# Performance work log

Hardware: AMD Instinct MI355X
Metric: run time of the kernel (lower is better)

Reference implementation:

```python
import jax, jax.numpy as jnp
import numpy as np

NUM_LAYERS = 2
DIM_Z = 128
NORM = float(np.sqrt(DIM_Z))
EPS = 1e-5


def _ln(v):
    # LayerNorm(elementwise_affine=False) over last dim
    m = v.mean(-1, keepdims=True)
    var = ((v - m) ** 2).mean(-1, keepdims=True)
    return (v - m) / jnp.sqrt(var + EPS)


def setup_inputs() -> dict:
    key = jax.random.key(0)
    ks = jax.random.split(key, 8)
    B, C, P = 32, 128, 128
    K, DS = 510, 256
    H = W = 64
    return {
        "x": jax.random.normal(ks[0], (B, C, P), jnp.float32),
        "latents": jax.random.normal(ks[1], (K, DS), jnp.float32),
        "blank_latent": jax.random.normal(ks[2], (NUM_LAYERS, DIM_Z), jnp.float32),
        "linear_w": jax.random.normal(ks[3], (DIM_Z, DS), jnp.float32) * 0.05,
        "linear_b": jnp.zeros((DIM_Z,), jnp.float32),
        "anchors_w": jax.random.normal(ks[4], (DIM_Z, C), jnp.float32) * 0.05,
        "anchors_b": jnp.zeros((DIM_Z,), jnp.float32),
        "prototypes": jax.random.uniform(ks[5], (K, 3, H, W), dtype=jnp.float32),
        "masks": jax.random.uniform(ks[6], (K, 1, H, W), dtype=jnp.float32),
    }


def reference(x, latents, blank_latent, linear_w, linear_b, anchors_w, anchors_b, prototypes, masks):
    B, C, P = x.shape
    L = NUM_LAYERS
    # codebook latents: (K, dim_sprites) -> Linear -> LN -> (K, dim_z)
    lat = _ln(latents @ linear_w.T + linear_b)
    xp = jnp.transpose(x, (0, 2, 1))                          # (B, P, C)
    a = _ln(xp.reshape(B * P, C) @ anchors_w.T + anchors_b)   # (B*P, dim_z)
    logits_main = a @ lat.T                                   # (B*P, K)
    # blank logits: position p uses blank_latent[p % L]; value repeated L times
    blank_pp = blank_latent[jnp.arange(P) % L]                # (P, dim_z == C)
    dots = jnp.einsum('bpc,pc->bp', xp, blank_pp)             # (B, P)
    logits_blank = jnp.broadcast_to(dots.reshape(B * P, 1), (B * P, L))
    logits = jnp.concatenate([logits_main, logits_blank], axis=-1) / NORM
    weights = jax.nn.softmax(logits, axis=-1)                 # (B*P, K+L)
    log_probs = jax.nn.log_softmax(
        jnp.transpose(logits.reshape(B, P, -1), (1, 0, 2)), axis=2)  # (P, B, K+L)
    # sprite bank: [prototypes;0] on rgb, [masks;0] on alpha -> (K+L, 4, H, W)
    zp = jnp.zeros((L,) + prototypes.shape[1:], prototypes.dtype)
    zm = jnp.zeros((L,) + masks.shape[1:], masks.dtype)
    sprite = jnp.concatenate(
        [jnp.concatenate([prototypes, zp], axis=0),
         jnp.concatenate([masks, zm], axis=0)], axis=1)
    # broadcast-multiply-reduce expressed as a single contraction
    S = jnp.einsum('nk,kchw->nchw', weights, sprite)          # (B*P, 4, H, W)
    H_, W_ = S.shape[-2], S.shape[-1]
    S_out = jnp.transpose(S.reshape(B, P, 4, H_, W_), (1, 0, 2, 3, 4))  # (P, B, 4, H, W)
    return (weights, logits, log_probs, S_out)
```

## Files before the change

### kernel.cpp

```cpp
#include <hip/hip_runtime.h>

typedef unsigned short u16;
typedef unsigned int u32;
typedef __bf16 bf16x8 __attribute__((ext_vector_type(8)));
typedef float f32x4 __attribute__((ext_vector_type(4)));

#define EPS 1e-5f
#define INV_NORM 0.088388347648318447f

#define OUT_W   0
#define OUT_LOG 2097152
#define OUT_LP  4194304
#define OUT_S   6291456

#define WS_BT   0
#define WS_LAT  8388608
#define WS_A    8454144

__device__ __forceinline__ u16 f2b(float f) {
  u32 i = __float_as_uint(f);
  return (u16)((i + 0x7FFFu + ((i >> 16) & 1u)) >> 16);
}
__device__ __forceinline__ float wsum(float v) {
#pragma unroll
  for (int off = 32; off > 0; off >>= 1) v += __shfl_down(v, off, 64);
  return v;
}
__device__ __forceinline__ float wmax(float v) {
#pragma unroll
  for (int off = 32; off > 0; off >>= 1) v = fmaxf(v, __shfl_down(v, off, 64));
  return v;
}
__device__ __forceinline__ float dot8(uint4 u, const float* xp) {
  float s;
  s  = xp[0] * __uint_as_float(u.x << 16);
  s += xp[1] * __uint_as_float(u.x & 0xFFFF0000u);
  s += xp[2] * __uint_as_float(u.y << 16);
  s += xp[3] * __uint_as_float(u.y & 0xFFFF0000u);
  s += xp[4] * __uint_as_float(u.z << 16);
  s += xp[5] * __uint_as_float(u.z & 0xFFFF0000u);
  s += xp[6] * __uint_as_float(u.w << 16);
  s += xp[7] * __uint_as_float(u.w & 0xFFFF0000u);
  return s;
}
__device__ __forceinline__ float dot4(float4 u, const float* xp) {
  return xp[0] * u.x + xp[1] * u.y + xp[2] * u.z + xp[3] * u.w;
}

__global__ __launch_bounds__(128) void k_lat(const float* __restrict__ latents,
                                             const float* __restrict__ lw,
                                             const float* __restrict__ lb,
                                             u16* __restrict__ latbf) {
  int k = blockIdx.x, t = threadIdx.x;
  int wid = t >> 6, lane = t & 63;
  __shared__ float ls[256];
  __shared__ float red[4];
  ls[t] = latents[k * 256 + t];
  ls[t + 128] = latents[k * 256 + 128 + t];
  __syncthreads();
  float v = lb[t];
  const float4* wv = (const float4*)(lw + t * 256);
#pragma unroll
  for (int c = 0; c < 64; c++) v += dot4(wv[c], &ls[c * 4]);
  float s = wsum(v), s2 = wsum(v * v);
  if (lane == 0) { red[wid * 2] = s; red[wid * 2 + 1] = s2; }
  __syncthreads();
  float mean = (red[0] + red[2]) * 0.0078125f;
  float var = (red[1] + red[3]) * 0.0078125f - mean * mean;
  latbf[k * 128 + t] = f2b((v - mean) * rsqrtf(var + EPS));
}

__global__ __launch_bounds__(256) void k_tr(const float* __restrict__ proto,
                                            const float* __restrict__ masks,
                                            u16* __restrict__ Bt) {
  __shared__ u16 tile[64 * 72];
  int t = threadIdx.x;
  int n0 = blockIdx.x * 64;
  int k0 = blockIdx.y * 64;
  int ch = n0 >> 12, hw0 = n0 & 4095;
  int r = t >> 2, c = (t & 3) * 16;
  int kg = k0 + r;
  u16 vals[16];
#pragma unroll
  for (int e = 0; e < 16; e++) vals[e] = 0;
  if (kg < 510) {
    const float* src = (ch < 3) ? (proto + ((size_t)kg * 3 + ch) * 4096 + hw0 + c)
                                : (masks + (size_t)kg * 4096 + hw0 + c);
    const float4* s4 = (const float4*)src;
#pragma unroll
    for (int q = 0; q < 4; q++) {
      float4 u = s4[q];
      vals[q * 4 + 0] = f2b(u.x);
      vals[q * 4 + 1] = f2b(u.y);
      vals[q * 4 + 2] = f2b(u.z);
      vals[q * 4 + 3] = f2b(u.w);
    }
  }
#pragma unroll
  for (int e = 0; e < 16; e++) tile[r * 72 + c + e] = vals[e];
  __syncthreads();
  int nr = t >> 2, kc = (t & 3) * 16;
  u32 u[8];
#pragma unroll
  for (int e = 0; e < 8; e++) {
    u32 lo = tile[(kc + 2 * e) * 72 + nr];
    u32 hi = tile[(kc + 2 * e + 1) * 72 + nr];
    u[e] = lo | (hi << 16);
  }
  u16* dst = Bt + (size_t)(n0 + nr) * 512 + k0 + kc;
  uint4 v0 = {u[0], u[1], u[2], u[3]};
  uint4 v1 = {u[4], u[5], u[6], u[7]};
  *(uint4*)dst = v0;
  *(uint4*)(dst + 8) = v1;
}

__global__ __launch_bounds__(128) void k_rows(const float* __restrict__ x,
                                              const float* __restrict__ aw,
                                              const float* __restrict__ ab,
                                              const float* __restrict__ blank,
                                              const u16* __restrict__ latbf,
                                              float* __restrict__ out,
                                              u16* __restrict__ Abf) {
  int n = blockIdx.x;
  int b = n >> 7, p = n & 127;
  int t = threadIdx.x, wid = t >> 6, lane = t & 63;
  __shared__ float xs[128];
  __shared__ float ash[128];
  __shared__ float red[8];
  xs[t] = x[(size_t)b * 16384 + (size_t)t * 128 + p];
  __syncthreads();
  float av = ab[t];
  const float4* awv = (const float4*)(aw + t * 128);
#pragma unroll
  for (int c = 0; c < 32; c++) av += dot4(awv[c], &xs[c * 4]);
  float bv = xs[t] * blank[(p & 1) * 128 + t];
  float s = wsum(av), s2 = wsum(av * av), sb = wsum(bv);
  if (lane == 0) { red[wid * 3] = s; red[wid * 3 + 1] = s2; red[wid * 3 + 2] = sb; }
  __syncthreads();
  float mean = (red[0] + red[3]) * 0.0078125f;
  float var = (red[1] + red[4]) * 0.0078125f - mean * mean;
  float dots = red[2] + red[5];
  float an = (av - mean) * rsqrtf(var + EPS);
  ash[t] = an;
  float bl = dots * INV_NORM;
  __syncthreads();
  const uint4* lv = (const uint4*)(latbf + (size_t)(4 * t) * 128);
  float a0 = 0.f, a1 = 0.f, a2 = 0.f, a3 = 0.f;
#pragma unroll
  for (int c = 0; c < 16; c++) {
    const float* ap = &ash[c * 8];
    a0 += dot8(lv[c], ap);
    a1 += dot8(lv[16 + c], ap);
    a2 += dot8(lv[32 + c], ap);
    a3 += dot8(lv[48 + c], ap);
  }
  float l[4];
  l[0] = a0 * INV_NORM;
  l[1] = a1 * INV_NORM;
  l[2] = (4 * t + 2 < 510) ? a2 * INV_NORM : bl;
  l[3] = (4 * t + 3 < 510) ? a3 * INV_NORM : bl;
  float lmax = fmaxf(fmaxf(l[0], l[1]), fmaxf(l[2], l[3]));
  float m = wmax(lmax);
  __syncthreads();
  if (lane == 0) red[wid] = m;
  __syncthreads();
  float M = fmaxf(red[0], red[1]);
  float se = 0.f;
#pragma unroll
  for (int i = 0; i < 4; i++) se += expf(l[i] - M);
  float ssum = wsum(se);
  __syncthreads();
  if (lane == 0) red[wid] = ssum;
  __syncthreads();
  float S = red[0] + red[1];
  float logZ = M + logf(S);
  size_t nb = (size_t)n * 512 + 4 * t;
  size_t lpb = (size_t)OUT_LP + ((size_t)p * 32 + b) * 512 + 4 * t;
  float4 wv4, lg4, lp4;
  u16 ab4[4];
  float* lpv = &lp4.x;
  float* wvv = &wv4.x;
  float* lgv = &lg4.x;
#pragma unroll
  for (int i = 0; i < 4; i++) {
    float lp = l[i] - logZ;
    float w = expf(lp);
    lpv[i] = lp;
    wvv[i] = w;
    lgv[i] = l[i];
    ab4[i] = f2b(w);
  }
  *(float4*)(out + OUT_W + nb) = wv4;
  *(float4*)(out + OUT_LOG + nb) = lg4;
  *(float4*)(out + lpb) = lp4;
  *(uint2*)(Abf + nb) = *(uint2*)ab4;
}

__global__ __launch_bounds__(256) void k_gemm(const u16* __restrict__ A,
                                              const u16* __restrict__ Bt,
                                              float* __restrict__ out) {
  __shared__ u16 As[128 * 64];
  __shared__ u16 Bs[128 * 64];
  int tid = threadIdx.x;
  int wid = tid >> 6, lane = tid & 63;
  int nBase = blockIdx.x * 128;
  int mBase = blockIdx.y * 128;
  int wm = wid >> 1, wn = wid & 1;
  int quad = lane >> 4, r16 = lane & 15;
  f32x4 acc[4][4];
#pragma unroll
  for (int i = 0; i < 4; i++)
#pragma unroll
    for (int j = 0; j < 4; j++) acc[i][j] = (f32x4){0.f, 0.f, 0.f, 0.f};

  int srow8 = wid * 8 + (lane >> 3);
  int kx = ((lane & 7) ^ (lane >> 3)) * 8;
  char* ldsA = (char*)As + wid * 1024;
  char* ldsB = (char*)Bs + wid * 1024;
  int sw = r16 & 7;

  for (int kt = 0; kt < 8; kt++) {
    int k0 = kt * 64;
#pragma unroll
    for (int q = 0; q < 4; q++) {
      int row = q * 32 + srow8;
      const u16* ga = A + (size_t)(mBase + row) * 512 + k0 + kx;
      const u16* gb = Bt + (size_t)(nBase + row) * 512 + k0 + kx;
      __builtin_amdgcn_global_load_lds(
          (__attribute__((address_space(1))) void*)ga,
          (__attribute__((address_space(3))) void*)(ldsA + q * 4096), 16, 0, 0);
      __builtin_amdgcn_global_load_lds(
          (__attribute__((address_space(1))) void*)gb,
          (__attribute__((address_space(3))) void*)(ldsB + q * 4096), 16, 0, 0);
    }
    __syncthreads();
#pragma unroll
    for (int kk = 0; kk < 2; kk++) {
      int ch = ((quad + 4 * kk) ^ sw) * 8;
      bf16x8 af[4], bfr[4];
#pragma unroll
      for (int i = 0; i < 4; i++)
        af[i] = *(const bf16x8*)&As[(wm * 64 + i * 16 + r16) * 64 + ch];
#pragma unroll
      for (int j = 0; j < 4; j++)
        bfr[j] = *(const bf16x8*)&Bs[(wn * 64 + j * 16 + r16) * 64 + ch];
#pragma unroll
      for (int i = 0; i < 4; i++)
#pragma unroll
        for (int j = 0; j < 4; j++)
          acc[i][j] = __builtin_amdgcn_mfma_f32_16x16x32_bf16(af[i], bfr[j],
                                                              acc[i][j], 0, 0, 0);
    }
    __syncthreads();
  }
#pragma unroll
  for (int i = 0; i < 4; i++) {
#pragma unroll
    for (int r = 0; r < 4; r++) {
      int mg = mBase + wm * 64 + i * 16 + quad * 4 + r;
      size_t orow = (size_t)((mg & 127) * 32 + (mg >> 7));
      float* orp = out + OUT_S + orow * 16384 + nBase + wn * 64 + r16;
#pragma unroll
      for (int j = 0; j < 4; j++) orp[j * 16] = acc[i][j][r];
    }
  }
}

extern "C" void kernel_launch(void* const* d_in, const int* in_sizes, int n_in,
                              void* d_out, int out_size, void* d_ws, size_t ws_size,
                              hipStream_t stream) {
  const float* x = (const float*)d_in[0];
  const float* latents = (const float*)d_in[1];
  const float* blank = (const float*)d_in[2];
  const float* lw = (const float*)d_in[3];
  const float* lb = (const float*)d_in[4];
  const float* aw = (const float*)d_in[5];
  const float* ab = (const float*)d_in[6];
  const float* proto = (const float*)d_in[7];
  const float* masks = (const float*)d_in[8];
  float* out = (float*)d_out;
  u16* ws16 = (u16*)d_ws;
  u16* Bt = ws16 + WS_BT;
  u16* latbf = ws16 + WS_LAT;
  u16* Abf = ws16 + WS_A;

  k_lat<<<510, 128, 0, stream>>>(latents, lw, lb, latbf);
  k_tr<<<dim3(256, 8), 256, 0, stream>>>(proto, masks, Bt);
  k_rows<<<4096, 128, 0, stream>>>(x, aw, ab, blank, latbf, out, Abf);
  k_gemm<<<dim3(128, 32), 256, 0, stream>>>(Abf, Bt, out);
}
```

Baseline: 515.1 us.

## Enlarge GEMM tiles to 256x256 with double-buffered LDS and XCD-aware block mapping

The sprite GEMM kernel moves from 128x128 tiles with 256 threads to 256x256 tiles with 512 threads, so each wave computes an 8x4 grid of MFMA blocks. The K loop now double-buffers A and B tiles in 128KB of dynamic LDS, prefetching the next K slice while computing the current one, and uses one barrier per iteration instead of two. Block indices are remapped so neighbouring tiles land on the same XCD, which should improve L2 reuse. The gains are better operand reuse and overlap of loads with compute. The costs are higher register pressure, lower occupancy from the large LDS footprint, and reliance on launching with more than 64KB of dynamic shared memory.

```diff
diff --git a/kernel.cpp b/kernel.cpp
--- a/kernel.cpp
+++ b/kernel.cpp
@@ -196,68 +196,79 @@
   *(uint2*)(Abf + nb) = *(uint2*)ab4;
 }
 
-__global__ __launch_bounds__(256) void k_gemm(const u16* __restrict__ A,
+__global__ __launch_bounds__(512) void k_gemm(const u16* __restrict__ A,
                                               const u16* __restrict__ Bt,
                                               float* __restrict__ out) {
-  __shared__ u16 As[128 * 64];
-  __shared__ u16 Bs[128 * 64];
+  extern __shared__ u16 lds[];
   int tid = threadIdx.x;
   int wid = tid >> 6, lane = tid & 63;
-  int nBase = blockIdx.x * 128;
-  int mBase = blockIdx.y * 128;
-  int wm = wid >> 1, wn = wid & 1;
+  int wm = wid >> 2, wn = wid & 3;
   int quad = lane >> 4, r16 = lane & 15;
-  f32x4 acc[4][4];
-#pragma unroll
-  for (int i = 0; i < 4; i++)
+
+  int wg = ((blockIdx.x & 7) << 7) | ((int)blockIdx.x >> 3);
+  int mb = wg & 15, nb = wg >> 4;
+  int mBase = mb << 8, nBase = nb << 8;
+
+  int srow = tid >> 3;
+  int kc8 = ((tid & 7) ^ (srow & 7)) << 3;
+  int sw = r16 & 7;
+  const size_t aRow = (size_t)(mBase + srow) * 512 + kc8;
+  const size_t bRow = (size_t)(nBase + srow) * 512 + kc8;
+
+  f32x4 acc[8][4];
+#pragma unroll
+  for (int i = 0; i < 8; i++)
 #pragma unroll
     for (int j = 0; j < 4; j++) acc[i][j] = (f32x4){0.f, 0.f, 0.f, 0.f};
 
-  int srow8 = wid * 8 + (lane >> 3);
-  int kx = ((lane & 7) ^ (lane >> 3)) * 8;
-  char* ldsA = (char*)As + wid * 1024;
-  char* ldsB = (char*)Bs + wid * 1024;
-  int sw = r16 & 7;
+#define STAGE(buf, kt) do {                                                     \
+    _Pragma("unroll")                                                           \
+    for (int q = 0; q < 4; q++) {                                               \
+      __builtin_amdgcn_global_load_lds(                                         \
+          (__attribute__((address_space(1))) void*)(A + aRow +                  \
+              (size_t)q * 32768 + (kt) * 64),                                   \
+          (__attribute__((address_space(3))) void*)((char*)lds +                \
+              (buf) * 65536 + q * 8192 + tid * 16), 16, 0, 0);                  \
+      __builtin_amdgcn_global_load_lds(                                         \
+          (__attribute__((address_space(1))) void*)(Bt + bRow +                 \
+              (size_t)q * 32768 + (kt) * 64),                                   \
+          (__attribute__((address_space(3))) void*)((char*)lds +                \
+              (buf) * 65536 + 32768 + q * 8192 + tid * 16), 16, 0, 0);          \
+    } } while (0)
+
+  STAGE(0, 0);
+  __syncthreads();
 
   for (int kt = 0; kt < 8; kt++) {
-    int k0 = kt * 64;
-#pragma unroll
-    for (int q = 0; q < 4; q++) {
-      int row = q * 32 + srow8;
-      const u16* ga = A + (size_t)(mBase + row) * 512 + k0 + kx;
-      const u16* gb = Bt + (size_t)(nBase + row) * 512 + k0 + kx;
-      __builtin_amdgcn_global_load_lds(
-          (__attribute__((address_space(1))) void*)ga,
-          (__attribute__((address_space(3))) void*)(ldsA + q * 4096), 16, 0, 0);
-      __builtin_amdgcn_global_load_lds(
-          (__attribute__((address_space(1))) void*)gb,
-          (__attribute__((address_space(3))) void*)(ldsB + q * 4096), 16, 0, 0);
+    int cur = kt & 1;
+    if (kt < 7) STAGE(cur ^ 1, kt + 1);
+    const u16* As_ = lds + cur * 32768;
+    const u16* Bs_ = As_ + 16384;
+#pragma unroll
+    for (int kk = 0; kk < 2; kk++) {
+      int ch = ((quad + 4 * kk) ^ sw) << 3;
+      bf16x8 bfr[4];
+#pragma unroll
+      for (int j = 0; j < 4; j++)
+        bfr[j] = *(const bf16x8*)&Bs_[(wn * 64 + j * 16 + r16) * 64 + ch];
+#pragma unroll
+      for (int i = 0; i < 8; i++) {
+        bf16x8 af = *(const bf16x8*)&As_[(wm * 128 + i * 16 + r16) * 64 + ch];
+#pragma unroll
+        for (int j = 0; j < 4; j++)
+          acc[i][j] = __builtin_amdgcn_mfma_f32_16x16x32_bf16(af, bfr[j],
+                                                              acc[i][j], 0, 0, 0);
+      }
     }
-    __syncthreads();
-#pragma unroll
-    for (int kk = 0; kk < 2; kk++) {
-      int ch = ((quad + 4 * kk) ^ sw) * 8;
-      bf16x8 af[4], bfr[4];
-#pragma unroll
-      for (int i = 0; i < 4; i++)
-        af[i] = *(const bf16x8*)&As[(wm * 64 + i * 16 + r16) * 64 + ch];
-#pragma unroll
-      for (int j = 0; j < 4; j++)
-        bfr[j] = *(const bf16x8*)&Bs[(wn * 64 + j * 16 + r16) * 64 + ch];
-#pragma unroll
-      for (int i = 0; i < 4; i++)
-#pragma unroll
-        for (int j = 0; j < 4; j++)
-          acc[i][j] = __builtin_amdgcn_mfma_f32_16x16x32_bf16(af[i], bfr[j],
-                                                              acc[i][j], 0, 0, 0);
-    }
-    __syncthreads();
-  }
-#pragma unroll
-  for (int i = 0; i < 4; i++) {
+    if (kt < 7) __syncthreads();
+  }
+#undef STAGE
+
+#pragma unroll
+  for (int i = 0; i < 8; i++) {
 #pragma unroll
     for (int r = 0; r < 4; r++) {
-      int mg = mBase + wm * 64 + i * 16 + quad * 4 + r;
+      int mg = mBase + wm * 128 + i * 16 + quad * 4 + r;
       size_t orow = (size_t)((mg & 127) * 32 + (mg >> 7));
       float* orp = out + OUT_S + orow * 16384 + nBase + wn * 64 + r16;
 #pragma unroll
@@ -287,5 +298,5 @@
   k_lat<<<510, 128, 0, stream>>>(latents, lw, lb, latbf);
   k_tr<<<dim3(256, 8), 256, 0, stream>>>(proto, masks, Bt);
   k_rows<<<4096, 128, 0, stream>>>(x, aw, ab, blank, latbf, out, Abf);
-  k_gemm<<<dim3(128, 32), 256, 0, stream>>>(Abf, Bt, out);
-}
+  k_gemm<<<1024, 512, 131072, stream>>>(Abf, Bt, out);
+}
```

New measurement: 504.4 us. 2.1% less time.
